# Performance work log

Hardware: AMD Instinct MI355X
Metric: run time of the kernel (lower is better)

## Reference

```python
import jax, jax.numpy as jnp
import numpy as np

N = 50000
IN_C, HID, OUT_C = 128, 64, 40


def setup_inputs() -> dict:
    key = jax.random.key(0)
    ks = jax.random.split(key, 10)
    x = jax.random.normal(ks[0], (N, IN_C), dtype=jnp.float32)
    edge_index = jax.random.randint(ks[1], (2, 1600000), 0, N, dtype=jnp.int64)
    edge_attr = jax.random.uniform(ks[2], (1600000,), dtype=jnp.float32)
    def lin(k, fan_in, fan_out):
        bound = 1.0 / np.sqrt(fan_in)
        return jax.random.uniform(k, (fan_in, fan_out), jnp.float32, -bound, bound)
    W1 = lin(ks[3], IN_C, HID); b1 = jnp.zeros((HID,), jnp.float32)
    W2 = lin(ks[4], HID, HID); b2 = jnp.zeros((HID,), jnp.float32)
    W3 = lin(ks[5], HID, OUT_C); b3 = jnp.zeros((OUT_C,), jnp.float32)
    return {"x": x, "edge_index": edge_index, "edge_attr": edge_attr,
            "W1": W1, "b1": b1, "W2": W2, "b2": b2, "W3": W3, "b3": b3}


def _gcn_conv(x, src, dst, norm, W, b):
    # h = x W ; out[i] = sum_{(j->i)} norm_e * h[j] ; + bias
    h = x @ W
    msg = norm[:, None] * h[src]          # [E+N, F_out] gathered messages
    out = jax.ops.segment_sum(msg, dst, num_segments=N)
    return out + b


def reference(x, edge_index, edge_attr, W1, b1, W2, b2, W3, b3):
    # GCN normalization with self-loops (fill_value=1), cached across layers.
    loops = jnp.arange(N, dtype=edge_index.dtype)
    src = jnp.concatenate([edge_index[0], loops])
    dst = jnp.concatenate([edge_index[1], loops])
    w = jnp.concatenate([edge_attr, jnp.ones((N,), edge_attr.dtype)])
    deg = jnp.zeros((N,), x.dtype).at[dst].add(w)
    dinv = jnp.where(deg > 0, jax.lax.rsqrt(deg), 0.0)
    norm = dinv[src] * w * dinv[dst]

    h = jax.nn.relu(_gcn_conv(x, src, dst, norm, W1, b1))   # dropout: eval no-op
    h = jax.nn.relu(_gcn_conv(h, src, dst, norm, W2, b2))
    h = jax.nn.relu(_gcn_conv(h, src, dst, norm, W3, b3))
    return jax.nn.log_softmax(h, axis=-1)
```

## Files before the change

kernel.cpp:

```cpp
#include <hip/hip_runtime.h>
#include <math.h>

#define N_NODES 50000
#define E_EDGES 1600000
#define IN_C    128
#define HID     64
#define OUT_C   40

#define BSH     9
#define BNODES  512
#define NB      98
#define CAP     20480
#define TILE    4096
#define P1T     512

typedef unsigned int uint;
typedef unsigned short ushort;

__device__ inline float b2f(ushort h) { return __uint_as_float(((uint)h) << 16); }
__device__ inline ushort f2b(float f) {
    uint u = __float_as_uint(f);
    u += 0x7FFFu + ((u >> 16) & 1u);
    return (ushort)(u >> 16);
}

__global__ __launch_bounds__(128) void k_zero_bc(int* __restrict__ bc) {
    if (threadIdx.x < NB) bc[threadIdx.x] = 0;
}

__global__ __launch_bounds__(P1T) void k_bin(const int* __restrict__ ei,
                                             const float* __restrict__ w,
                                             int* __restrict__ bcursor,
                                             uint2* __restrict__ tmp) {
    __shared__ uint2 stage[TILE];
    __shared__ unsigned char sbuck[TILE];
    __shared__ int hist[NB], startb[NB], cursor[NB], baseg[NB];
    __shared__ int sc[128];
    const int tid = threadIdx.x;
    const int e0  = blockIdx.x * TILE;
    const int n   = min(TILE, E_EDGES - e0);

    for (int i = tid; i < NB; i += P1T) hist[i] = 0;
    __syncthreads();

    for (int i = tid; i < n; i += P1T) {
        int d = ei[E_EDGES + e0 + i];
        atomicAdd(&hist[d >> BSH], 1);
    }
    __syncthreads();

    if (tid < 128) sc[tid] = (tid < NB) ? hist[tid] : 0;
    __syncthreads();
    for (int off = 1; off < 128; off <<= 1) {
        int x = 0;
        if (tid < 128 && tid >= off) x = sc[tid - off];
        __syncthreads();
        if (tid < 128) sc[tid] += x;
        __syncthreads();
    }
    if (tid < NB) {
        int st = sc[tid] - hist[tid];
        startb[tid] = st;
        cursor[tid] = st;
        baseg[tid]  = atomicAdd(&bcursor[tid], hist[tid]);
    }
    __syncthreads();

    for (int i = tid; i < n; i += P1T) {
        int   s  = ei[e0 + i];
        int   d  = ei[E_EDGES + e0 + i];
        float wv = w[e0 + i];
        int   b  = d >> BSH;
        int pos = atomicAdd(&cursor[b], 1);
        stage[pos] = make_uint2(((uint)(d & (BNODES - 1)) << 16) | (uint)s,
                                __float_as_uint(wv));
        sbuck[pos] = (unsigned char)b;
    }
    __syncthreads();

    for (int i = tid; i < n; i += P1T) {
        int b = sbuck[i];
        int gpos = baseg[b] + (i - startb[b]);
        tmp[(size_t)b * CAP + gpos] = stage[i];
    }
}

__global__ __launch_bounds__(128) void k_bucket_scan(const int* __restrict__ bcursor,
                                                     int* __restrict__ ebase,
                                                     int* __restrict__ rowptr) {
    __shared__ int s[128];
    int t = threadIdx.x;
    int v = (t < NB) ? bcursor[t] : 0;
    s[t] = v;
    __syncthreads();
    for (int off = 1; off < 128; off <<= 1) {
        int x = (t >= off) ? s[t - off] : 0;
        __syncthreads();
        s[t] += x;
        __syncthreads();
    }
    if (t < NB) ebase[t] = s[t] - v;
    if (t == 0) rowptr[N_NODES] = E_EDGES;
}

__global__ __launch_bounds__(BNODES) void k_build(const int* __restrict__ bcursor,
                                                  const int* __restrict__ ebase,
                                                  const uint2* __restrict__ tmp,
                                                  int* __restrict__ rowptr,
                                                  float* __restrict__ dinv,
                                                  uint2* __restrict__ csr) {
    __shared__ int   hist[BNODES];
    __shared__ float wsum[BNODES];
    __shared__ int   sc[BNODES];
    const int tid = threadIdx.x;
    const int b   = blockIdx.x;
    const int cnt = bcursor[b];
    const int eb  = ebase[b];
    const uint2* tb = tmp + (size_t)b * CAP;

    hist[tid] = 0; wsum[tid] = 0.0f;
    __syncthreads();
    for (int i = tid; i < cnt; i += BNODES) {
        uint2 u = tb[i];
        int dl = u.x >> 16;
        atomicAdd(&hist[dl], 1);
        atomicAdd(&wsum[dl], __uint_as_float(u.y));
    }
    __syncthreads();

    int own = hist[tid];
    sc[tid] = own;
    __syncthreads();
    for (int off = 1; off < BNODES; off <<= 1) {
        int x = (tid >= off) ? sc[tid - off] : 0;
        __syncthreads();
        sc[tid] += x;
        __syncthreads();
    }
    int excl = sc[tid] - own;
    int node = (b << BSH) + tid;
    if (node < N_NODES) {
        rowptr[node] = eb + excl;
        dinv[node]   = rsqrtf(1.0f + wsum[tid]);
    }
    hist[tid] = excl;
    __syncthreads();

    for (int i = tid; i < cnt; i += BNODES) {
        uint2 u = tb[i];
        int dl = u.x >> 16;
        int pos = atomicAdd(&hist[dl], 1);
        csr[eb + pos] = make_uint2(u.x & 0xFFFFu, u.y);
    }
}

__global__ __launch_bounds__(256) void k_gemm1(const float* __restrict__ x,
                                               const float* __restrict__ W,
                                               const float* __restrict__ dinv,
                                               ushort* __restrict__ g) {
    __shared__ float s_x[4 * IN_C];
    const int tid = threadIdx.x;
    const int base = blockIdx.x * 4;
    for (int idx = tid; idx < 4 * IN_C; idx += 256)
        s_x[idx] = x[(size_t)base * IN_C + idx];
    __syncthreads();
    const int node = base + (tid >> 6);
    const int f = tid & 63;
    const float* row = &s_x[(tid >> 6) * IN_C];
    float acc = 0.0f;
#pragma unroll 8
    for (int k = 0; k < IN_C; ++k) acc += row[k] * W[k * HID + f];
    g[(size_t)node * HID + f] = f2b(dinv[node] * acc);
}

template <int F_OUT>
__global__ __launch_bounds__(256) void k_agg_gemm(const int* __restrict__ rowptr,
                                                  const uint2* __restrict__ csr,
                                                  const ushort* __restrict__ g,
                                                  const float* __restrict__ dinv,
                                                  const float* __restrict__ bias,
                                                  const float* __restrict__ W,
                                                  ushort* __restrict__ g_next) {
    __shared__ float s_act[4][HID];
    const int tid  = threadIdx.x;
    const int wv   = tid >> 6;
    const int lane = tid & 63;
    const int node = blockIdx.x * 4 + wv;
    const int grp  = lane >> 4;
    const int sub  = lane & 15;
    const int beg = rowptr[node], end = rowptr[node + 1];

    float4 acc; acc.x = acc.y = acc.z = acc.w = 0.0f;
    if (grp == 0) {
        ushort4 v = ((const ushort4*)(g + (size_t)node * HID))[sub];
        acc.x = b2f(v.x); acc.y = b2f(v.y); acc.z = b2f(v.z); acc.w = b2f(v.w);
    }

    int e = beg;
    for (; e + 8 <= end; e += 8) {
        uint2 ed0 = csr[e + grp], ed1 = csr[e + 4 + grp];
        ushort4 v0 = ((const ushort4*)(g + (size_t)ed0.x * HID))[sub];
        ushort4 v1 = ((const ushort4*)(g + (size_t)ed1.x * HID))[sub];
        float w0 = __uint_as_float(ed0.y), w1 = __uint_as_float(ed1.y);
        acc.x += w0 * b2f(v0.x) + w1 * b2f(v1.x);
        acc.y += w0 * b2f(v0.y) + w1 * b2f(v1.y);
        acc.z += w0 * b2f(v0.z) + w1 * b2f(v1.z);
        acc.w += w0 * b2f(v0.w) + w1 * b2f(v1.w);
    }
    for (; e < end; e += 4) {
        int myE = e + grp;
        bool a = myE < end;
        uint2 ed = csr[a ? myE : beg];
        float wN = a ? __uint_as_float(ed.y) : 0.0f;
        ushort4 v = ((const ushort4*)(g + (size_t)ed.x * HID))[sub];
        acc.x += wN * b2f(v.x); acc.y += wN * b2f(v.y);
        acc.z += wN * b2f(v.z); acc.w += wN * b2f(v.w);
    }
#pragma unroll
    for (int m = 16; m <= 32; m <<= 1) {
        acc.x += __shfl_xor(acc.x, m); acc.y += __shfl_xor(acc.y, m);
        acc.z += __shfl_xor(acc.z, m); acc.w += __shfl_xor(acc.w, m);
    }
    if (grp == 0) {
        float dv = dinv[node];
        float4 b4 = ((const float4*)bias)[sub];
        float4 v;
        v.x = fmaxf(dv * acc.x + b4.x, 0.0f);
        v.y = fmaxf(dv * acc.y + b4.y, 0.0f);
        v.z = fmaxf(dv * acc.z + b4.z, 0.0f);
        v.w = fmaxf(dv * acc.w + b4.w, 0.0f);
        ((float4*)&s_act[wv][0])[sub] = v;
    }
    __syncthreads();
    if (lane < F_OUT) {
        float dot = 0.0f;
#pragma unroll
        for (int k = 0; k < HID; ++k) dot += s_act[wv][k] * W[k * F_OUT + lane];
        g_next[(size_t)node * F_OUT + lane] = f2b(dinv[node] * dot);
    }
}

__global__ __launch_bounds__(256) void k_final_agg(const int* __restrict__ rowptr,
                                                   const uint2* __restrict__ csr,
                                                   const ushort* __restrict__ g,
                                                   const float* __restrict__ dinv,
                                                   const float* __restrict__ bias,
                                                   float* __restrict__ out) {
    const int tid  = threadIdx.x;
    const int wv   = tid >> 6;
    const int lane = tid & 63;
    const int node = blockIdx.x * 4 + wv;
    const int grp  = lane >> 4;
    const int sub  = lane & 15;
    const bool live = sub < (OUT_C / 4);
    const int beg = rowptr[node], end = rowptr[node + 1];

    float4 acc; acc.x = acc.y = acc.z = acc.w = 0.0f;
    if (grp == 0 && live) {
        ushort4 v = ((const ushort4*)(g + (size_t)node * OUT_C))[sub];
        acc.x = b2f(v.x); acc.y = b2f(v.y); acc.z = b2f(v.z); acc.w = b2f(v.w);
    }

    int e = beg;
    for (; e + 8 <= end; e += 8) {
        uint2 ed0 = csr[e + grp], ed1 = csr[e + 4 + grp];
        if (live) {
            ushort4 v0 = ((const ushort4*)(g + (size_t)ed0.x * OUT_C))[sub];
            ushort4 v1 = ((const ushort4*)(g + (size_t)ed1.x * OUT_C))[sub];
            float w0 = __uint_as_float(ed0.y), w1 = __uint_as_float(ed1.y);
            acc.x += w0 * b2f(v0.x) + w1 * b2f(v1.x);
            acc.y += w0 * b2f(v0.y) + w1 * b2f(v1.y);
            acc.z += w0 * b2f(v0.z) + w1 * b2f(v1.z);
            acc.w += w0 * b2f(v0.w) + w1 * b2f(v1.w);
        }
    }
    for (; e < end; e += 4) {
        int myE = e + grp;
        bool a = myE < end;
        uint2 ed = csr[a ? myE : beg];
        float wN = a ? __uint_as_float(ed.y) : 0.0f;
        if (live) {
            ushort4 v = ((const ushort4*)(g + (size_t)ed.x * OUT_C))[sub];
            acc.x += wN * b2f(v.x); acc.y += wN * b2f(v.y);
            acc.z += wN * b2f(v.z); acc.w += wN * b2f(v.w);
        }
    }
#pragma unroll
    for (int m = 16; m <= 32; m <<= 1) {
        acc.x += __shfl_xor(acc.x, m); acc.y += __shfl_xor(acc.y, m);
        acc.z += __shfl_xor(acc.z, m); acc.w += __shfl_xor(acc.w, m);
    }

    float dv = dinv[node];
    float4 v; v.x = v.y = v.z = v.w = 0.0f;
    bool own = (grp == 0) && live;
    if (own) {
        float4 b4 = ((const float4*)bias)[sub];
        v.x = fmaxf(dv * acc.x + b4.x, 0.0f);
        v.y = fmaxf(dv * acc.y + b4.y, 0.0f);
        v.z = fmaxf(dv * acc.z + b4.z, 0.0f);
        v.w = fmaxf(dv * acc.w + b4.w, 0.0f);
    }
    float m = own ? fmaxf(fmaxf(v.x, v.y), fmaxf(v.z, v.w)) : -INFINITY;
#pragma unroll
    for (int off = 1; off < 16; off <<= 1) m = fmaxf(m, __shfl_xor(m, off));
    float s = own ? (expf(v.x - m) + expf(v.y - m) + expf(v.z - m) + expf(v.w - m)) : 0.0f;
#pragma unroll
    for (int off = 1; off < 16; off <<= 1) s += __shfl_xor(s, off);
    if (own) {
        float lg = m + logf(s);
        float4 o;
        o.x = v.x - lg; o.y = v.y - lg; o.z = v.z - lg; o.w = v.w - lg;
        ((float4*)&out[(size_t)node * OUT_C])[sub] = o;
    }
}

extern "C" void kernel_launch(void* const* d_in, const int* in_sizes, int n_in,
                              void* d_out, int out_size, void* d_ws, size_t ws_size,
                              hipStream_t stream) {
    const float* x  = (const float*)d_in[0];
    const int*   ei = (const int*)d_in[1];
    const float* w  = (const float*)d_in[2];
    const float* W1 = (const float*)d_in[3];
    const float* b1 = (const float*)d_in[4];
    const float* W2 = (const float*)d_in[5];
    const float* b2 = (const float*)d_in[6];
    const float* W3 = (const float*)d_in[7];
    const float* b3 = (const float*)d_in[8];
    float* out = (float*)d_out;

    char* ws = (char*)d_ws;
    size_t off = 0;
    auto carve = [&](size_t bytes) {
        char* p = ws + off;
        off += (bytes + 255) & ~(size_t)255;
        return p;
    };
    int*   bcursor = (int*)carve(NB * sizeof(int));
    int*   ebase   = (int*)carve(NB * sizeof(int));
    int*   rowptr  = (int*)carve((N_NODES + 1) * sizeof(int));
    float* dinv    = (float*)carve(N_NODES * sizeof(float));
    uint2* csr     = (uint2*)carve((size_t)E_EDGES * sizeof(uint2));
    uint2* tmp     = (uint2*)carve((size_t)NB * CAP * sizeof(uint2));
    ushort* g1 = (ushort*)tmp;
    ushort* g2 = g1 + (size_t)N_NODES * HID;
    ushort* g3 = g1;
    (void)ws_size;

    const int nbBin = (E_EDGES + TILE - 1) / TILE;
    const int nbN4  = N_NODES / 4;

    k_zero_bc<<<1, 128, 0, stream>>>(bcursor);
    k_bin<<<nbBin, P1T, 0, stream>>>(ei, w, bcursor, tmp);
    k_bucket_scan<<<1, 128, 0, stream>>>(bcursor, ebase, rowptr);
    k_build<<<NB, BNODES, 0, stream>>>(bcursor, ebase, tmp, rowptr, dinv, csr);

    k_gemm1<<<nbN4, 256, 0, stream>>>(x, W1, dinv, g1);
    k_agg_gemm<HID><<<nbN4, 256, 0, stream>>>(rowptr, csr, g1, dinv, b1, W2, g2);
    k_agg_gemm<OUT_C><<<nbN4, 256, 0, stream>>>(rowptr, csr, g2, dinv, b2, W3, g3);
    k_final_agg<<<nbN4, 256, 0, stream>>>(rowptr, csr, g3, dinv, b3, out);
}
```

Baseline: 277.7 us.

## Pack CSR edges to 32-bit, fuse bucket scan, stage weights in LDS, prefetch edges

Packs each CSR entry into one 32-bit word (16-bit source index plus bf16 weight), halving edge-list traffic in the three aggregation kernels. The bucket scan moves into k_build, and the zeroing kernel becomes a memset, which removes two small launches. The first-layer GEMM and the fused agg-GEMM kernels now stage their weight matrices in shared memory, and gemm1 processes 16 nodes per block. The aggregation loops load 16 edges at a time, broadcast them by shuffle, prefetch the next batch, and split the sum across two accumulators. Rounding edge weights to bf16 adds precision loss, and the 16-bit source index relies on a src<65536 encoding that was already present.

```diff
diff --git a/kernel.cpp b/kernel.cpp
--- a/kernel.cpp
+++ b/kernel.cpp
@@ -13,6 +13,7 @@
 #define CAP     20480
 #define TILE    4096
 #define P1T     512
+#define NPB     16
 
 typedef unsigned int uint;
 typedef unsigned short ushort;
@@ -22,10 +23,6 @@
     uint u = __float_as_uint(f);
     u += 0x7FFFu + ((u >> 16) & 1u);
     return (ushort)(u >> 16);
-}
-
-__global__ __launch_bounds__(128) void k_zero_bc(int* __restrict__ bc) {
-    if (threadIdx.x < NB) bc[threadIdx.x] = 0;
 }
 
 __global__ __launch_bounds__(P1T) void k_bin(const int* __restrict__ ei,
@@ -85,41 +82,34 @@
     }
 }
 
-__global__ __launch_bounds__(128) void k_bucket_scan(const int* __restrict__ bcursor,
-                                                     int* __restrict__ ebase,
-                                                     int* __restrict__ rowptr) {
-    __shared__ int s[128];
-    int t = threadIdx.x;
-    int v = (t < NB) ? bcursor[t] : 0;
-    s[t] = v;
-    __syncthreads();
-    for (int off = 1; off < 128; off <<= 1) {
-        int x = (t >= off) ? s[t - off] : 0;
-        __syncthreads();
-        s[t] += x;
-        __syncthreads();
-    }
-    if (t < NB) ebase[t] = s[t] - v;
-    if (t == 0) rowptr[N_NODES] = E_EDGES;
-}
-
 __global__ __launch_bounds__(BNODES) void k_build(const int* __restrict__ bcursor,
-                                                  const int* __restrict__ ebase,
                                                   const uint2* __restrict__ tmp,
                                                   int* __restrict__ rowptr,
                                                   float* __restrict__ dinv,
-                                                  uint2* __restrict__ csr) {
+                                                  uint* __restrict__ csr) {
     __shared__ int   hist[BNODES];
     __shared__ float wsum[BNODES];
     __shared__ int   sc[BNODES];
+    __shared__ int   sb[128];
+    __shared__ int   s_eb;
     const int tid = threadIdx.x;
     const int b   = blockIdx.x;
+
+    if (tid < 128) sb[tid] = (tid < NB) ? bcursor[tid] : 0;
+    hist[tid] = 0; wsum[tid] = 0.0f;
+    __syncthreads();
+    for (int off = 1; off < 128; off <<= 1) {
+        int x = (tid < 128 && tid >= off) ? sb[tid - off] : 0;
+        __syncthreads();
+        if (tid < 128) sb[tid] += x;
+        __syncthreads();
+    }
+    if (tid == 0) s_eb = sb[b] - bcursor[b];
+    __syncthreads();
     const int cnt = bcursor[b];
-    const int eb  = ebase[b];
+    const int eb  = s_eb;
     const uint2* tb = tmp + (size_t)b * CAP;
 
-    hist[tid] = 0; wsum[tid] = 0.0f;
-    __syncthreads();
     for (int i = tid; i < cnt; i += BNODES) {
         uint2 u = tb[i];
         int dl = u.x >> 16;
@@ -143,6 +133,7 @@
         rowptr[node] = eb + excl;
         dinv[node]   = rsqrtf(1.0f + wsum[tid]);
     }
+    if (b == 0 && tid == 0) rowptr[N_NODES] = E_EDGES;
     hist[tid] = excl;
     __syncthreads();
 
@@ -150,7 +141,7 @@
         uint2 u = tb[i];
         int dl = u.x >> 16;
         int pos = atomicAdd(&hist[dl], 1);
-        csr[eb + pos] = make_uint2(u.x & 0xFFFFu, u.y);
+        csr[eb + pos] = ((uint)f2b(__uint_as_float(u.y)) << 16) | (u.x & 0xFFFFu);
     }
 }
 
@@ -158,31 +149,46 @@
                                                const float* __restrict__ W,
                                                const float* __restrict__ dinv,
                                                ushort* __restrict__ g) {
-    __shared__ float s_x[4 * IN_C];
+    __shared__ float sW[IN_C * HID];
+    __shared__ float sx[NPB * IN_C];
     const int tid = threadIdx.x;
-    const int base = blockIdx.x * 4;
-    for (int idx = tid; idx < 4 * IN_C; idx += 256)
-        s_x[idx] = x[(size_t)base * IN_C + idx];
-    __syncthreads();
-    const int node = base + (tid >> 6);
-    const int f = tid & 63;
-    const float* row = &s_x[(tid >> 6) * IN_C];
-    float acc = 0.0f;
+    const size_t base = (size_t)blockIdx.x * NPB;
+
+    for (int i = tid; i < (IN_C * HID) / 4; i += 256)
+        ((float4*)sW)[i] = ((const float4*)W)[i];
+    for (int i = tid; i < (NPB * IN_C) / 4; i += 256)
+        ((float4*)sx)[i] = ((const float4*)(x + base * IN_C))[i];
+    __syncthreads();
+
+    const int wv = tid >> 6, f = tid & 63;
+    for (int nn = 0; nn < 4; ++nn) {
+        const int nl = wv * 4 + nn;
+        const float* row = &sx[nl * IN_C];
+        float acc = 0.0f;
 #pragma unroll 8
-    for (int k = 0; k < IN_C; ++k) acc += row[k] * W[k * HID + f];
-    g[(size_t)node * HID + f] = f2b(dinv[node] * acc);
+        for (int k = 0; k < IN_C; k += 4) {
+            float4 a = *(const float4*)&row[k];
+            acc += a.x * sW[(k + 0) * HID + f] + a.y * sW[(k + 1) * HID + f]
+                 + a.z * sW[(k + 2) * HID + f] + a.w * sW[(k + 3) * HID + f];
+        }
+        const size_t node = base + nl;
+        g[node * HID + f] = f2b(dinv[node] * acc);
+    }
 }
 
 template <int F_OUT>
 __global__ __launch_bounds__(256) void k_agg_gemm(const int* __restrict__ rowptr,
-                                                  const uint2* __restrict__ csr,
+                                                  const uint* __restrict__ csr,
                                                   const ushort* __restrict__ g,
                                                   const float* __restrict__ dinv,
                                                   const float* __restrict__ bias,
                                                   const float* __restrict__ W,
                                                   ushort* __restrict__ g_next) {
+    __shared__ float sW[HID * F_OUT];
     __shared__ float s_act[4][HID];
     const int tid  = threadIdx.x;
+    for (int i = tid; i < HID * F_OUT; i += 256) sW[i] = W[i];
+
     const int wv   = tid >> 6;
     const int lane = tid & 63;
     const int node = blockIdx.x * 4 + wv;
@@ -190,58 +196,65 @@
     const int sub  = lane & 15;
     const int beg = rowptr[node], end = rowptr[node + 1];
 
-    float4 acc; acc.x = acc.y = acc.z = acc.w = 0.0f;
+    float4 acc0, acc1;
+    acc0.x = acc0.y = acc0.z = acc0.w = 0.0f;
+    acc1 = acc0;
     if (grp == 0) {
         ushort4 v = ((const ushort4*)(g + (size_t)node * HID))[sub];
-        acc.x = b2f(v.x); acc.y = b2f(v.y); acc.z = b2f(v.z); acc.w = b2f(v.w);
-    }
-
-    int e = beg;
-    for (; e + 8 <= end; e += 8) {
-        uint2 ed0 = csr[e + grp], ed1 = csr[e + 4 + grp];
-        ushort4 v0 = ((const ushort4*)(g + (size_t)ed0.x * HID))[sub];
-        ushort4 v1 = ((const ushort4*)(g + (size_t)ed1.x * HID))[sub];
-        float w0 = __uint_as_float(ed0.y), w1 = __uint_as_float(ed1.y);
-        acc.x += w0 * b2f(v0.x) + w1 * b2f(v1.x);
-        acc.y += w0 * b2f(v0.y) + w1 * b2f(v1.y);
-        acc.z += w0 * b2f(v0.z) + w1 * b2f(v1.z);
-        acc.w += w0 * b2f(v0.w) + w1 * b2f(v1.w);
-    }
-    for (; e < end; e += 4) {
-        int myE = e + grp;
-        bool a = myE < end;
-        uint2 ed = csr[a ? myE : beg];
-        float wN = a ? __uint_as_float(ed.y) : 0.0f;
-        ushort4 v = ((const ushort4*)(g + (size_t)ed.x * HID))[sub];
-        acc.x += wN * b2f(v.x); acc.y += wN * b2f(v.y);
-        acc.z += wN * b2f(v.z); acc.w += wN * b2f(v.w);
-    }
+        acc0.x = b2f(v.x); acc0.y = b2f(v.y); acc0.z = b2f(v.z); acc0.w = b2f(v.w);
+    }
+
+    uint curd = csr[min(beg + sub, E_EDGES - 1)];
+    for (int e = beg; e < end; e += 16) {
+        uint nextd = csr[min(e + 16 + sub, E_EDGES - 1)];
+#pragma unroll
+        for (int i = 0; i < 4; ++i) {
+            uint d = __shfl(curd, (grp << 4) + 4 * i + grp);
+            bool valid = (e + 4 * i + grp) < end;
+            float wv2 = valid ? b2f((ushort)(d >> 16)) : 0.0f;
+            int srcn = (int)(d & 0xFFFFu);
+            ushort4 v = ((const ushort4*)(g + (size_t)srcn * HID))[sub];
+            if (i & 1) {
+                acc1.x += wv2 * b2f(v.x); acc1.y += wv2 * b2f(v.y);
+                acc1.z += wv2 * b2f(v.z); acc1.w += wv2 * b2f(v.w);
+            } else {
+                acc0.x += wv2 * b2f(v.x); acc0.y += wv2 * b2f(v.y);
+                acc0.z += wv2 * b2f(v.z); acc0.w += wv2 * b2f(v.w);
+            }
+        }
+        curd = nextd;
+    }
+    acc0.x += acc1.x; acc0.y += acc1.y; acc0.z += acc1.z; acc0.w += acc1.w;
 #pragma unroll
     for (int m = 16; m <= 32; m <<= 1) {
-        acc.x += __shfl_xor(acc.x, m); acc.y += __shfl_xor(acc.y, m);
-        acc.z += __shfl_xor(acc.z, m); acc.w += __shfl_xor(acc.w, m);
+        acc0.x += __shfl_xor(acc0.x, m); acc0.y += __shfl_xor(acc0.y, m);
+        acc0.z += __shfl_xor(acc0.z, m); acc0.w += __shfl_xor(acc0.w, m);
     }
     if (grp == 0) {
         float dv = dinv[node];
         float4 b4 = ((const float4*)bias)[sub];
         float4 v;
-        v.x = fmaxf(dv * acc.x + b4.x, 0.0f);
-        v.y = fmaxf(dv * acc.y + b4.y, 0.0f);
-        v.z = fmaxf(dv * acc.z + b4.z, 0.0f);
-        v.w = fmaxf(dv * acc.w + b4.w, 0.0f);
+        v.x = fmaxf(dv * acc0.x + b4.x, 0.0f);
+        v.y = fmaxf(dv * acc0.y + b4.y, 0.0f);
+        v.z = fmaxf(dv * acc0.z + b4.z, 0.0f);
+        v.w = fmaxf(dv * acc0.w + b4.w, 0.0f);
         ((float4*)&s_act[wv][0])[sub] = v;
     }
     __syncthreads();
     if (lane < F_OUT) {
         float dot = 0.0f;
-#pragma unroll
-        for (int k = 0; k < HID; ++k) dot += s_act[wv][k] * W[k * F_OUT + lane];
+#pragma unroll 4
+        for (int k = 0; k < HID; k += 4) {
+            float4 a = *(const float4*)&s_act[wv][k];
+            dot += a.x * sW[(k + 0) * F_OUT + lane] + a.y * sW[(k + 1) * F_OUT + lane]
+                 + a.z * sW[(k + 2) * F_OUT + lane] + a.w * sW[(k + 3) * F_OUT + lane];
+        }
         g_next[(size_t)node * F_OUT + lane] = f2b(dinv[node] * dot);
     }
 }
 
 __global__ __launch_bounds__(256) void k_final_agg(const int* __restrict__ rowptr,
-                                                   const uint2* __restrict__ csr,
+                                                   const uint* __restrict__ csr,
                                                    const ushort* __restrict__ g,
                                                    const float* __restrict__ dinv,
                                                    const float* __restrict__ bias,
@@ -255,40 +268,41 @@
     const bool live = sub < (OUT_C / 4);
     const int beg = rowptr[node], end = rowptr[node + 1];
 
-    float4 acc; acc.x = acc.y = acc.z = acc.w = 0.0f;
+    float4 acc0, acc1;
+    acc0.x = acc0.y = acc0.z = acc0.w = 0.0f;
+    acc1 = acc0;
     if (grp == 0 && live) {
         ushort4 v = ((const ushort4*)(g + (size_t)node * OUT_C))[sub];
-        acc.x = b2f(v.x); acc.y = b2f(v.y); acc.z = b2f(v.z); acc.w = b2f(v.w);
-    }
-
-    int e = beg;
-    for (; e + 8 <= end; e += 8) {
-        uint2 ed0 = csr[e + grp], ed1 = csr[e + 4 + grp];
-        if (live) {
-            ushort4 v0 = ((const ushort4*)(g + (size_t)ed0.x * OUT_C))[sub];
-            ushort4 v1 = ((const ushort4*)(g + (size_t)ed1.x * OUT_C))[sub];
-            float w0 = __uint_as_float(ed0.y), w1 = __uint_as_float(ed1.y);
-            acc.x += w0 * b2f(v0.x) + w1 * b2f(v1.x);
-            acc.y += w0 * b2f(v0.y) + w1 * b2f(v1.y);
-            acc.z += w0 * b2f(v0.z) + w1 * b2f(v1.z);
-            acc.w += w0 * b2f(v0.w) + w1 * b2f(v1.w);
+        acc0.x = b2f(v.x); acc0.y = b2f(v.y); acc0.z = b2f(v.z); acc0.w = b2f(v.w);
+    }
+
+    uint curd = csr[min(beg + sub, E_EDGES - 1)];
+    for (int e = beg; e < end; e += 16) {
+        uint nextd = csr[min(e + 16 + sub, E_EDGES - 1)];
+#pragma unroll
+        for (int i = 0; i < 4; ++i) {
+            uint d = __shfl(curd, (grp << 4) + 4 * i + grp);
+            bool valid = (e + 4 * i + grp) < end;
+            float wv2 = valid ? b2f((ushort)(d >> 16)) : 0.0f;
+            int srcn = (int)(d & 0xFFFFu);
+            if (live) {
+                ushort4 v = ((const ushort4*)(g + (size_t)srcn * OUT_C))[sub];
+                if (i & 1) {
+                    acc1.x += wv2 * b2f(v.x); acc1.y += wv2 * b2f(v.y);
+                    acc1.z += wv2 * b2f(v.z); acc1.w += wv2 * b2f(v.w);
+                } else {
+                    acc0.x += wv2 * b2f(v.x); acc0.y += wv2 * b2f(v.y);
+                    acc0.z += wv2 * b2f(v.z); acc0.w += wv2 * b2f(v.w);
+                }
+            }
         }
-    }
-    for (; e < end; e += 4) {
-        int myE = e + grp;
-        bool a = myE < end;
-        uint2 ed = csr[a ? myE : beg];
-        float wN = a ? __uint_as_float(ed.y) : 0.0f;
-        if (live) {
-            ushort4 v = ((const ushort4*)(g + (size_t)ed.x * OUT_C))[sub];
-            acc.x += wN * b2f(v.x); acc.y += wN * b2f(v.y);
-            acc.z += wN * b2f(v.z); acc.w += wN * b2f(v.w);
-        }
-    }
+        curd = nextd;
+    }
+    acc0.x += acc1.x; acc0.y += acc1.y; acc0.z += acc1.z; acc0.w += acc1.w;
 #pragma unroll
     for (int m = 16; m <= 32; m <<= 1) {
-        acc.x += __shfl_xor(acc.x, m); acc.y += __shfl_xor(acc.y, m);
-        acc.z += __shfl_xor(acc.z, m); acc.w += __shfl_xor(acc.w, m);
+        acc0.x += __shfl_xor(acc0.x, m); acc0.y += __shfl_xor(acc0.y, m);
+        acc0.z += __shfl_xor(acc0.z, m); acc0.w += __shfl_xor(acc0.w, m);
     }
 
     float dv = dinv[node];
@@ -296,10 +310,10 @@
     bool own = (grp == 0) && live;
     if (own) {
         float4 b4 = ((const float4*)bias)[sub];
-        v.x = fmaxf(dv * acc.x + b4.x, 0.0f);
-        v.y = fmaxf(dv * acc.y + b4.y, 0.0f);
-        v.z = fmaxf(dv * acc.z + b4.z, 0.0f);
-        v.w = fmaxf(dv * acc.w + b4.w, 0.0f);
+        v.x = fmaxf(dv * acc0.x + b4.x, 0.0f);
+        v.y = fmaxf(dv * acc0.y + b4.y, 0.0f);
+        v.z = fmaxf(dv * acc0.z + b4.z, 0.0f);
+        v.w = fmaxf(dv * acc0.w + b4.w, 0.0f);
     }
     float m = own ? fmaxf(fmaxf(v.x, v.y), fmaxf(v.z, v.w)) : -INFINITY;
 #pragma unroll
@@ -337,10 +351,9 @@
         return p;
     };
     int*   bcursor = (int*)carve(NB * sizeof(int));
-    int*   ebase   = (int*)carve(NB * sizeof(int));
     int*   rowptr  = (int*)carve((N_NODES + 1) * sizeof(int));
     float* dinv    = (float*)carve(N_NODES * sizeof(float));
-    uint2* csr     = (uint2*)carve((size_t)E_EDGES * sizeof(uint2));
+    uint*  csr     = (uint*)carve((size_t)E_EDGES * sizeof(uint));
     uint2* tmp     = (uint2*)carve((size_t)NB * CAP * sizeof(uint2));
     ushort* g1 = (ushort*)tmp;
     ushort* g2 = g1 + (size_t)N_NODES * HID;
@@ -349,13 +362,13 @@
 
     const int nbBin = (E_EDGES + TILE - 1) / TILE;
     const int nbN4  = N_NODES / 4;
-
-    k_zero_bc<<<1, 128, 0, stream>>>(bcursor);
+    const int nbG1  = N_NODES / NPB;
+
+    hipMemsetAsync(bcursor, 0, NB * sizeof(int), stream);
     k_bin<<<nbBin, P1T, 0, stream>>>(ei, w, bcursor, tmp);
-    k_bucket_scan<<<1, 128, 0, stream>>>(bcursor, ebase, rowptr);
-    k_build<<<NB, BNODES, 0, stream>>>(bcursor, ebase, tmp, rowptr, dinv, csr);
-
-    k_gemm1<<<nbN4, 256, 0, stream>>>(x, W1, dinv, g1);
+    k_build<<<NB, BNODES, 0, stream>>>(bcursor, tmp, rowptr, dinv, csr);
+
+    k_gemm1<<<nbG1, 256, 0, stream>>>(x, W1, dinv, g1);
     k_agg_gemm<HID><<<nbN4, 256, 0, stream>>>(rowptr, csr, g1, dinv, b1, W2, g2);
     k_agg_gemm<OUT_C><<<nbN4, 256, 0, stream>>>(rowptr, csr, g2, dinv, b2, W3, g3);
     k_final_agg<<<nbN4, 256, 0, stream>>>(rowptr, csr, g3, dinv, b3, out);
```

Result: faster. 253.6 us (-8.7%).
